# Kernel optimization log

Hardware: AMD Instinct MI355X
Metric: run time of the kernel (lower is better)

Reference implementation:

```python
import jax, jax.numpy as jnp
import numpy as np

B, C, H, W = 512, 32, 16, 16
HEADS = 8
D = C * H * W // HEADS  # 1024, per-head flattened dim; Linear is square (D -> D)
W_SCALE = 0.002


def setup_inputs() -> dict:
    key = jax.random.key(0)
    ks = jax.random.split(key, 9)
    f32 = jnp.float32
    return {
        "query": jax.random.normal(ks[0], (B, C, H, W), f32),
        "key": jax.random.normal(ks[1], (B, C, H, W), f32),
        "value": jax.random.normal(ks[2], (B, C, H, W), f32),
        # stacked per-head Linear params: W* is (heads, out=D, in=D) like torch Linear weight
        "W1": jax.random.normal(ks[3], (HEADS, D, D), f32) * W_SCALE,
        "b1": jax.random.normal(ks[4], (HEADS, D), f32) * W_SCALE,
        "W2": jax.random.normal(ks[5], (HEADS, D, D), f32) * W_SCALE,
        "b2": jax.random.normal(ks[6], (HEADS, D), f32) * W_SCALE,
        "W3": jax.random.normal(ks[7], (HEADS, D, D), f32) * W_SCALE,
        "b3": jax.random.normal(ks[8], (HEADS, D), f32) * W_SCALE,
    }


def reference(query, key, value, W1, b1, W2, b2, W3, b3):
    b, c, h, w = query.shape
    heads, d, _ = W1.shape
    # chunk over channels + flatten per head: (b, heads, d)
    q = query.reshape(b, heads, d)
    k = key.reshape(b, heads, d)
    v = value.reshape(b, heads, d)
    # per-head square Linear projections (torch: x @ W.T + b)
    q = jnp.einsum("nhd,hed->nhe", q, W1) + b1
    k = jnp.einsum("nhd,hed->nhe", k, W2) + b2
    v = jnp.einsum("nhd,hed->nhe", v, W3) + b3
    # original divides by p = 1/sqrt(d), i.e. multiplies scores by sqrt(d)
    scale = jnp.sqrt(jnp.asarray(d, q.dtype))
    scores = jnp.einsum("nhe,mhe->hnm", q, k) * scale  # (heads, b, b) attention over batch
    attn = jax.nn.softmax(scores, axis=-1)
    out = jnp.einsum("hnm,mhe->nhe", attn, v)  # (b, heads, d)
    return out.reshape(b, c, h, w)
```

## Files before the change

### kernel.cpp

```cpp
#include <hip/hip_runtime.h>

typedef _Float16 half8 __attribute__((ext_vector_type(8)));
typedef float f32x4 __attribute__((ext_vector_type(4)));

namespace {

constexpr int HEADS = 8;
constexpr int BATCH = 512;
constexpr int DH    = 1024;
constexpr int CHW   = HEADS * DH;

constexpr int BM = 128, BN = 128, BK = 32;
constexpr int LDW = BK + 8;

__device__ __forceinline__ int xcd_swz(int bid, int nwg) {
  const int q = nwg >> 3;
  return (bid & 7) * q + (bid >> 3);
}

__device__ __forceinline__ half8 cvt8(float4 a, float4 b) {
  half8 r;
  r[0] = (_Float16)a.x; r[1] = (_Float16)a.y; r[2] = (_Float16)a.z; r[3] = (_Float16)a.w;
  r[4] = (_Float16)b.x; r[5] = (_Float16)b.y; r[6] = (_Float16)b.z; r[7] = (_Float16)b.w;
  return r;
}

__global__ __launch_bounds__(256) void proj_kernel(
    const float* __restrict__ Xq, const float* __restrict__ Xk, const float* __restrict__ Xv,
    const float* __restrict__ W1, const float* __restrict__ b1,
    const float* __restrict__ W2, const float* __restrict__ b2,
    const float* __restrict__ W3, const float* __restrict__ b3,
    _Float16* __restrict__ Qp, _Float16* __restrict__ Kp, _Float16* __restrict__ VpT) {
  __shared__ _Float16 As[2][BM * LDW];
  __shared__ _Float16 Bs[2][BN * LDW];
  const int tid = threadIdx.x;
  const int l  = xcd_swz(blockIdx.x, 768);
  const int z  = l >> 8, rem = l & 255;
  const int h  = rem >> 5, bx = rem & 31;
  const int tm = bx & 3, tn = bx >> 2;
  const float* X    = (z == 0) ? Xq : (z == 1) ? Xk : Xv;
  const float* W    = (z == 0) ? W1 : (z == 1) ? W2 : W3;
  const float* bias = (z == 0) ? b1 : (z == 1) ? b2 : b3;
  _Float16*    P    = (z == 0) ? Qp : (z == 1) ? Kp : VpT;

  const int lane = tid & 63, w = tid >> 6;
  const int wr = (w >> 1) * 64, wc = (w & 1) * 64;
  const int lr = lane & 15, lk = lane >> 4;
  const int srow = tid >> 1, sc0 = (tid & 1) * 16;

  const float* ga = X + (size_t)(tm * BM + srow) * CHW + (size_t)h * DH + sc0;
  const float* gb = W + (size_t)h * DH * DH + (size_t)(tn * BN + srow) * DH + sc0;

  constexpr int NT = DH / BK;
  float4 ra0, ra1, ra2, ra3, rb0, rb1, rb2, rb3;
  ra0 = ((const float4*)ga)[0]; ra1 = ((const float4*)ga)[1];
  ra2 = ((const float4*)ga)[2]; ra3 = ((const float4*)ga)[3];
  rb0 = ((const float4*)gb)[0]; rb1 = ((const float4*)gb)[1];
  rb2 = ((const float4*)gb)[2]; rb3 = ((const float4*)gb)[3];
  ga += BK; gb += BK;
  *(half8*)&As[0][srow * LDW + sc0]     = cvt8(ra0, ra1);
  *(half8*)&As[0][srow * LDW + sc0 + 8] = cvt8(ra2, ra3);
  *(half8*)&Bs[0][srow * LDW + sc0]     = cvt8(rb0, rb1);
  *(half8*)&Bs[0][srow * LDW + sc0 + 8] = cvt8(rb2, rb3);
  ra0 = ((const float4*)ga)[0]; ra1 = ((const float4*)ga)[1];
  ra2 = ((const float4*)ga)[2]; ra3 = ((const float4*)ga)[3];
  rb0 = ((const float4*)gb)[0]; rb1 = ((const float4*)gb)[1];
  rb2 = ((const float4*)gb)[2]; rb3 = ((const float4*)gb)[3];
  ga += BK; gb += BK;
  __syncthreads();

  f32x4 acc[4][4] = {};
  int c = 0;
#pragma unroll 1
  for (int t = 0; t < NT; ++t) {
    const _Float16* Ac = As[c];
    const _Float16* Bc = Bs[c];
    half8 av[4], bv[4];
#pragma unroll
    for (int i = 0; i < 4; ++i)
      av[i] = *(const half8*)&Ac[(wr + i * 16 + lr) * LDW + lk * 8];
#pragma unroll
    for (int j = 0; j < 4; ++j)
      bv[j] = *(const half8*)&Bc[(wc + j * 16 + lr) * LDW + lk * 8];
    if (t + 1 < NT) {
      _Float16* An = As[c ^ 1];
      _Float16* Bn = Bs[c ^ 1];
      *(half8*)&An[srow * LDW + sc0]     = cvt8(ra0, ra1);
      *(half8*)&An[srow * LDW + sc0 + 8] = cvt8(ra2, ra3);
      *(half8*)&Bn[srow * LDW + sc0]     = cvt8(rb0, rb1);
      *(half8*)&Bn[srow * LDW + sc0 + 8] = cvt8(rb2, rb3);
      if (t + 2 < NT) {
        ra0 = ((const float4*)ga)[0]; ra1 = ((const float4*)ga)[1];
        ra2 = ((const float4*)ga)[2]; ra3 = ((const float4*)ga)[3];
        rb0 = ((const float4*)gb)[0]; rb1 = ((const float4*)gb)[1];
        rb2 = ((const float4*)gb)[2]; rb3 = ((const float4*)gb)[3];
        ga += BK; gb += BK;
      }
    }
#pragma unroll
    for (int i = 0; i < 4; ++i)
#pragma unroll
      for (int j = 0; j < 4; ++j)
        acc[i][j] = __builtin_amdgcn_mfma_f32_16x16x32_f16(av[i], bv[j], acc[i][j], 0, 0, 0);
    __syncthreads();
    c ^= 1;
  }

#pragma unroll
  for (int i = 0; i < 4; ++i)
#pragma unroll
    for (int j = 0; j < 4; ++j) {
      const int e = tn * BN + wc + j * 16 + lr;
      const float bb = bias[h * DH + e];
#pragma unroll
      for (int q = 0; q < 4; ++q) {
        const int n = tm * BM + wr + i * 16 + lk * 4 + q;
        const float val = acc[i][j][q] + bb;
        if (z != 2) P[((size_t)h * BATCH + n) * DH + e] = (_Float16)val;
        else        P[((size_t)h * DH + e) * BATCH + n] = (_Float16)val;
      }
    }
}

template <int NT>
__device__ __forceinline__ void gemm_f16_core(
    const _Float16* ga, const _Float16* gb,
    _Float16 (*As)[BM * LDW], _Float16 (*Bs)[BN * LDW],
    int srow, int sc0, int wr, int wc, int lr, int lk, f32x4 (&acc)[4][4]) {
  half8 rA0 = ((const half8*)ga)[0], rA1 = ((const half8*)ga)[1];
  half8 rB0 = ((const half8*)gb)[0], rB1 = ((const half8*)gb)[1];
  ga += BK; gb += BK;
  *(half8*)&As[0][srow * LDW + sc0]     = rA0;
  *(half8*)&As[0][srow * LDW + sc0 + 8] = rA1;
  *(half8*)&Bs[0][srow * LDW + sc0]     = rB0;
  *(half8*)&Bs[0][srow * LDW + sc0 + 8] = rB1;
  rA0 = ((const half8*)ga)[0]; rA1 = ((const half8*)ga)[1];
  rB0 = ((const half8*)gb)[0]; rB1 = ((const half8*)gb)[1];
  ga += BK; gb += BK;
  __syncthreads();

  int c = 0;
#pragma unroll 1
  for (int t = 0; t < NT; ++t) {
    const _Float16* Ac = As[c];
    const _Float16* Bc = Bs[c];
    half8 av[4], bv[4];
#pragma unroll
    for (int i = 0; i < 4; ++i)
      av[i] = *(const half8*)&Ac[(wr + i * 16 + lr) * LDW + lk * 8];
#pragma unroll
    for (int j = 0; j < 4; ++j)
      bv[j] = *(const half8*)&Bc[(wc + j * 16 + lr) * LDW + lk * 8];
    if (t + 1 < NT) {
      _Float16* An = As[c ^ 1];
      _Float16* Bn = Bs[c ^ 1];
      *(half8*)&An[srow * LDW + sc0]     = rA0;
      *(half8*)&An[srow * LDW + sc0 + 8] = rA1;
      *(half8*)&Bn[srow * LDW + sc0]     = rB0;
      *(half8*)&Bn[srow * LDW + sc0 + 8] = rB1;
      if (t + 2 < NT) {
        rA0 = ((const half8*)ga)[0]; rA1 = ((const half8*)ga)[1];
        rB0 = ((const half8*)gb)[0]; rB1 = ((const half8*)gb)[1];
        ga += BK; gb += BK;
      }
    }
#pragma unroll
    for (int i = 0; i < 4; ++i)
#pragma unroll
      for (int j = 0; j < 4; ++j)
        acc[i][j] = __builtin_amdgcn_mfma_f32_16x16x32_f16(av[i], bv[j], acc[i][j], 0, 0, 0);
    __syncthreads();
    c ^= 1;
  }
}

__global__ __launch_bounds__(256) void score_kernel(
    const _Float16* __restrict__ Qp, const _Float16* __restrict__ Kp,
    float* __restrict__ S) {
  __shared__ _Float16 As[2][BM * LDW];
  __shared__ _Float16 Bs[2][BN * LDW];
  const int tid = threadIdx.x;
  const int l  = xcd_swz(blockIdx.x, 128);
  const int h  = l >> 4, bx = l & 15;
  const int tm = bx & 3, tn = bx >> 2;
  const int lane = tid & 63, w = tid >> 6;
  const int wr = (w >> 1) * 64, wc = (w & 1) * 64;
  const int lr = lane & 15, lk = lane >> 4;
  const int srow = tid >> 1, sc0 = (tid & 1) * 16;

  const _Float16* ga = Qp + ((size_t)h * BATCH + tm * BM + srow) * DH + sc0;
  const _Float16* gb = Kp + ((size_t)h * BATCH + tn * BN + srow) * DH + sc0;

  f32x4 acc[4][4] = {};
  gemm_f16_core<DH / BK>(ga, gb, As, Bs, srow, sc0, wr, wc, lr, lk, acc);

#pragma unroll
  for (int i = 0; i < 4; ++i)
#pragma unroll
    for (int j = 0; j < 4; ++j) {
      const int m = tn * BN + wc + j * 16 + lr;
#pragma unroll
      for (int q = 0; q < 4; ++q) {
        const int n = tm * BM + wr + i * 16 + lk * 4 + q;
        S[((size_t)h * BATCH + n) * BATCH + m] = 32.0f * acc[i][j][q];
      }
    }
}

__global__ __launch_bounds__(64) void softmax_kernel(
    const float* __restrict__ S, _Float16* __restrict__ A) {
  const size_t r = (size_t)blockIdx.x * BATCH;
  const int l = threadIdx.x;
  float v[8];
  float mx = -1e30f;
#pragma unroll
  for (int i = 0; i < 8; ++i) { v[i] = S[r + i * 64 + l]; mx = fmaxf(mx, v[i]); }
#pragma unroll
  for (int off = 32; off; off >>= 1) mx = fmaxf(mx, __shfl_xor(mx, off));
  float sum = 0.f;
#pragma unroll
  for (int i = 0; i < 8; ++i) { v[i] = __expf(v[i] - mx); sum += v[i]; }
#pragma unroll
  for (int off = 32; off; off >>= 1) sum += __shfl_xor(sum, off);
  const float inv = 1.f / sum;
#pragma unroll
  for (int i = 0; i < 8; ++i) A[r + i * 64 + l] = (_Float16)(v[i] * inv);
}

__global__ __launch_bounds__(256) void pv_kernel(
    const _Float16* __restrict__ At, const _Float16* __restrict__ VpT,
    float* __restrict__ Out) {
  __shared__ _Float16 As[2][BM * LDW];
  __shared__ _Float16 Bs[2][BN * LDW];
  const int tid = threadIdx.x;
  const int l  = xcd_swz(blockIdx.x, 256);
  const int h  = l >> 5, bx = l & 31;
  const int tm = bx & 3, tn = bx >> 2;
  const int lane = tid & 63, w = tid >> 6;
  const int wr = (w >> 1) * 64, wc = (w & 1) * 64;
  const int lr = lane & 15, lk = lane >> 4;
  const int srow = tid >> 1, sc0 = (tid & 1) * 16;

  const _Float16* ga = At  + ((size_t)h * BATCH + tm * BM + srow) * BATCH + sc0;
  const _Float16* gb = VpT + ((size_t)h * DH   + tn * BN + srow) * BATCH + sc0;

  f32x4 acc[4][4] = {};
  gemm_f16_core<BATCH / BK>(ga, gb, As, Bs, srow, sc0, wr, wc, lr, lk, acc);

#pragma unroll
  for (int i = 0; i < 4; ++i)
#pragma unroll
    for (int j = 0; j < 4; ++j) {
      const int e = tn * BN + wc + j * 16 + lr;
#pragma unroll
      for (int q = 0; q < 4; ++q) {
        const int n = tm * BM + wr + i * 16 + lk * 4 + q;
        Out[((size_t)n * HEADS + h) * DH + e] = acc[i][j][q];
      }
    }
}

}

extern "C" void kernel_launch(void* const* d_in, const int* in_sizes, int n_in,
                              void* d_out, int out_size, void* d_ws, size_t ws_size,
                              hipStream_t stream) {
  (void)in_sizes; (void)n_in; (void)out_size; (void)ws_size;
  const float* q  = (const float*)d_in[0];
  const float* k  = (const float*)d_in[1];
  const float* v  = (const float*)d_in[2];
  const float* W1 = (const float*)d_in[3];
  const float* b1 = (const float*)d_in[4];
  const float* W2 = (const float*)d_in[5];
  const float* b2 = (const float*)d_in[6];
  const float* W3 = (const float*)d_in[7];
  const float* b3 = (const float*)d_in[8];
  float* out = (float*)d_out;

  _Float16* Qp  = (_Float16*)d_ws;
  _Float16* Kp  = Qp + (size_t)BATCH * HEADS * DH;
  _Float16* VpT = Kp + (size_t)BATCH * HEADS * DH;
  float*    S   = (float*)(VpT + (size_t)BATCH * HEADS * DH);
  _Float16* At  = (_Float16*)(S + (size_t)HEADS * BATCH * BATCH);

  const dim3 blk(256);
  proj_kernel<<<dim3(768), blk, 0, stream>>>(q, k, v, W1, b1, W2, b2, W3, b3, Qp, Kp, VpT);
  score_kernel<<<dim3(128), blk, 0, stream>>>(Qp, Kp, S);
  softmax_kernel<<<dim3(HEADS * BATCH), dim3(64), 0, stream>>>(S, At);
  pv_kernel<<<dim3(256), blk, 0, stream>>>(At, VpT, out);
}
```

Before: 108.2 us.

## Use direct global-to-LDS loads with XOR-swizzled single-buffer tiles in all GEMMs

Replaces the register-staged, double-buffered LDS fill in the projection, score and PV GEMMs with global_load_lds 16-byte direct copies into an XOR-swizzled single-buffer tile. The projection kernel now stores fp32 tiles in LDS and converts to fp16 when reading fragments. The fp16 GEMMs move to a K tile of 64 with two MFMAs per fragment pair. This is meant to cut VGPR staging, LDS bank conflicts and loop overhead. In exchange it loses the overlap of the next tile's global load with compute, since each iteration loads then waits behind two barriers.

```diff
diff --git a/kernel.cpp b/kernel.cpp
--- a/kernel.cpp
+++ b/kernel.cpp
@@ -10,12 +10,17 @@
 constexpr int DH    = 1024;
 constexpr int CHW   = HEADS * DH;
 
-constexpr int BM = 128, BN = 128, BK = 32;
-constexpr int LDW = BK + 8;
+constexpr int BM = 128, BN = 128;
 
 __device__ __forceinline__ int xcd_swz(int bid, int nwg) {
   const int q = nwg >> 3;
   return (bid & 7) * q + (bid >> 3);
+}
+
+typedef __attribute__((address_space(3))) unsigned int lds_u32;
+typedef const __attribute__((address_space(1))) unsigned int glb_u32;
+__device__ __forceinline__ void gl_lds16(const void* g, void* l) {
+  __builtin_amdgcn_global_load_lds((glb_u32*)g, (lds_u32*)l, 16, 0, 0);
 }
 
 __device__ __forceinline__ half8 cvt8(float4 a, float4 b) {
@@ -31,8 +36,8 @@
     const float* __restrict__ W2, const float* __restrict__ b2,
     const float* __restrict__ W3, const float* __restrict__ b3,
     _Float16* __restrict__ Qp, _Float16* __restrict__ Kp, _Float16* __restrict__ VpT) {
-  __shared__ _Float16 As[2][BM * LDW];
-  __shared__ _Float16 Bs[2][BN * LDW];
+  __shared__ __align__(16) float As[BM * 32];
+  __shared__ __align__(16) float Bs[BN * 32];
   const int tid = threadIdx.x;
   const int l  = xcd_swz(blockIdx.x, 768);
   const int z  = l >> 8, rem = l & 255;
@@ -46,64 +51,57 @@
   const int lane = tid & 63, w = tid >> 6;
   const int wr = (w >> 1) * 64, wc = (w & 1) * 64;
   const int lr = lane & 15, lk = lane >> 4;
-  const int srow = tid >> 1, sc0 = (tid & 1) * 16;
-
-  const float* ga = X + (size_t)(tm * BM + srow) * CHW + (size_t)h * DH + sc0;
-  const float* gb = W + (size_t)h * DH * DH + (size_t)(tn * BN + srow) * DH + sc0;
-
-  constexpr int NT = DH / BK;
-  float4 ra0, ra1, ra2, ra3, rb0, rb1, rb2, rb3;
-  ra0 = ((const float4*)ga)[0]; ra1 = ((const float4*)ga)[1];
-  ra2 = ((const float4*)ga)[2]; ra3 = ((const float4*)ga)[3];
-  rb0 = ((const float4*)gb)[0]; rb1 = ((const float4*)gb)[1];
-  rb2 = ((const float4*)gb)[2]; rb3 = ((const float4*)gb)[3];
-  ga += BK; gb += BK;
-  *(half8*)&As[0][srow * LDW + sc0]     = cvt8(ra0, ra1);
-  *(half8*)&As[0][srow * LDW + sc0 + 8] = cvt8(ra2, ra3);
-  *(half8*)&Bs[0][srow * LDW + sc0]     = cvt8(rb0, rb1);
-  *(half8*)&Bs[0][srow * LDW + sc0 + 8] = cvt8(rb2, rb3);
-  ra0 = ((const float4*)ga)[0]; ra1 = ((const float4*)ga)[1];
-  ra2 = ((const float4*)ga)[2]; ra3 = ((const float4*)ga)[3];
-  rb0 = ((const float4*)gb)[0]; rb1 = ((const float4*)gb)[1];
-  rb2 = ((const float4*)gb)[2]; rb3 = ((const float4*)gb)[3];
-  ga += BK; gb += BK;
-  __syncthreads();
-
+
+  const char* Ab = (const char*)(X + (size_t)tm * BM * CHW + (size_t)h * DH);
+  const char* Bb = (const char*)(W + (size_t)h * DH * DH + (size_t)tn * BN * DH);
+
+  const char* srcA0; const char* srcA1; const char* srcA2; const char* srcA3;
+  const char* srcB0; const char* srcB1; const char* srcB2; const char* srcB3;
+  int off0, off1, off2, off3;
+  {
+    int off, row, scb;
+    off = 0 * 4096 + tid * 16; row = off >> 7; scb = ((off >> 4) & 7) ^ (row & 7);
+    off0 = off; srcA0 = Ab + (size_t)row * (CHW * 4) + scb * 16; srcB0 = Bb + (size_t)row * (DH * 4) + scb * 16;
+    off = 1 * 4096 + tid * 16; row = off >> 7; scb = ((off >> 4) & 7) ^ (row & 7);
+    off1 = off; srcA1 = Ab + (size_t)row * (CHW * 4) + scb * 16; srcB1 = Bb + (size_t)row * (DH * 4) + scb * 16;
+    off = 2 * 4096 + tid * 16; row = off >> 7; scb = ((off >> 4) & 7) ^ (row & 7);
+    off2 = off; srcA2 = Ab + (size_t)row * (CHW * 4) + scb * 16; srcB2 = Bb + (size_t)row * (DH * 4) + scb * 16;
+    off = 3 * 4096 + tid * 16; row = off >> 7; scb = ((off >> 4) & 7) ^ (row & 7);
+    off3 = off; srcA3 = Ab + (size_t)row * (CHW * 4) + scb * 16; srcB3 = Bb + (size_t)row * (DH * 4) + scb * 16;
+  }
+
+  constexpr int NT = DH / 32;
   f32x4 acc[4][4] = {};
-  int c = 0;
 #pragma unroll 1
   for (int t = 0; t < NT; ++t) {
-    const _Float16* Ac = As[c];
-    const _Float16* Bc = Bs[c];
+    __syncthreads();
+    gl_lds16(srcA0, (char*)As + off0); gl_lds16(srcB0, (char*)Bs + off0);
+    gl_lds16(srcA1, (char*)As + off1); gl_lds16(srcB1, (char*)Bs + off1);
+    gl_lds16(srcA2, (char*)As + off2); gl_lds16(srcB2, (char*)Bs + off2);
+    gl_lds16(srcA3, (char*)As + off3); gl_lds16(srcB3, (char*)Bs + off3);
+    srcA0 += 128; srcA1 += 128; srcA2 += 128; srcA3 += 128;
+    srcB0 += 128; srcB1 += 128; srcB2 += 128; srcB3 += 128;
+    __syncthreads();
     half8 av[4], bv[4];
 #pragma unroll
-    for (int i = 0; i < 4; ++i)
-      av[i] = *(const half8*)&Ac[(wr + i * 16 + lr) * LDW + lk * 8];
-#pragma unroll
-    for (int j = 0; j < 4; ++j)
-      bv[j] = *(const half8*)&Bc[(wc + j * 16 + lr) * LDW + lk * 8];
-    if (t + 1 < NT) {
-      _Float16* An = As[c ^ 1];
-      _Float16* Bn = Bs[c ^ 1];
-      *(half8*)&An[srow * LDW + sc0]     = cvt8(ra0, ra1);
-      *(half8*)&An[srow * LDW + sc0 + 8] = cvt8(ra2, ra3);
-      *(half8*)&Bn[srow * LDW + sc0]     = cvt8(rb0, rb1);
-      *(half8*)&Bn[srow * LDW + sc0 + 8] = cvt8(rb2, rb3);
-      if (t + 2 < NT) {
-        ra0 = ((const float4*)ga)[0]; ra1 = ((const float4*)ga)[1];
-        ra2 = ((const float4*)ga)[2]; ra3 = ((const float4*)ga)[3];
-        rb0 = ((const float4*)gb)[0]; rb1 = ((const float4*)gb)[1];
-        rb2 = ((const float4*)gb)[2]; rb3 = ((const float4*)gb)[3];
-        ga += BK; gb += BK;
-      }
+    for (int i = 0; i < 4; ++i) {
+      const int row = wr + i * 16 + lr;
+      const float4 p0 = *(const float4*)&As[row * 32 + (((lk * 2)    ) ^ (row & 7)) * 4];
+      const float4 p1 = *(const float4*)&As[row * 32 + (((lk * 2 + 1)) ^ (row & 7)) * 4];
+      av[i] = cvt8(p0, p1);
+    }
+#pragma unroll
+    for (int j = 0; j < 4; ++j) {
+      const int row = wc + j * 16 + lr;
+      const float4 p0 = *(const float4*)&Bs[row * 32 + (((lk * 2)    ) ^ (row & 7)) * 4];
+      const float4 p1 = *(const float4*)&Bs[row * 32 + (((lk * 2 + 1)) ^ (row & 7)) * 4];
+      bv[j] = cvt8(p0, p1);
     }
 #pragma unroll
     for (int i = 0; i < 4; ++i)
 #pragma unroll
       for (int j = 0; j < 4; ++j)
         acc[i][j] = __builtin_amdgcn_mfma_f32_16x16x32_f16(av[i], bv[j], acc[i][j], 0, 0, 0);
-    __syncthreads();
-    c ^= 1;
   }
 
 #pragma unroll
@@ -123,62 +121,63 @@
 }
 
 template <int NT>
-__device__ __forceinline__ void gemm_f16_core(
-    const _Float16* ga, const _Float16* gb,
-    _Float16 (*As)[BM * LDW], _Float16 (*Bs)[BN * LDW],
-    int srow, int sc0, int wr, int wc, int lr, int lk, f32x4 (&acc)[4][4]) {
-  half8 rA0 = ((const half8*)ga)[0], rA1 = ((const half8*)ga)[1];
-  half8 rB0 = ((const half8*)gb)[0], rB1 = ((const half8*)gb)[1];
-  ga += BK; gb += BK;
-  *(half8*)&As[0][srow * LDW + sc0]     = rA0;
-  *(half8*)&As[0][srow * LDW + sc0 + 8] = rA1;
-  *(half8*)&Bs[0][srow * LDW + sc0]     = rB0;
-  *(half8*)&Bs[0][srow * LDW + sc0 + 8] = rB1;
-  rA0 = ((const half8*)ga)[0]; rA1 = ((const half8*)ga)[1];
-  rB0 = ((const half8*)gb)[0]; rB1 = ((const half8*)gb)[1];
-  ga += BK; gb += BK;
-  __syncthreads();
-
-  int c = 0;
+__device__ __forceinline__ void gemm16_core(
+    const char* ga, size_t lda, const char* gb, size_t ldb,
+    _Float16* As, _Float16* Bs,
+    int tid, int wr, int wc, int lr, int lk, f32x4 (&acc)[4][4]) {
+  const char* srcA0; const char* srcA1; const char* srcA2; const char* srcA3;
+  const char* srcB0; const char* srcB1; const char* srcB2; const char* srcB3;
+  int off0, off1, off2, off3;
+  {
+    int off, row, scb;
+    off = 0 * 4096 + tid * 16; row = off >> 7; scb = ((off >> 4) & 7) ^ (row & 7);
+    off0 = off; srcA0 = ga + (size_t)row * lda + scb * 16; srcB0 = gb + (size_t)row * ldb + scb * 16;
+    off = 1 * 4096 + tid * 16; row = off >> 7; scb = ((off >> 4) & 7) ^ (row & 7);
+    off1 = off; srcA1 = ga + (size_t)row * lda + scb * 16; srcB1 = gb + (size_t)row * ldb + scb * 16;
+    off = 2 * 4096 + tid * 16; row = off >> 7; scb = ((off >> 4) & 7) ^ (row & 7);
+    off2 = off; srcA2 = ga + (size_t)row * lda + scb * 16; srcB2 = gb + (size_t)row * ldb + scb * 16;
+    off = 3 * 4096 + tid * 16; row = off >> 7; scb = ((off >> 4) & 7) ^ (row & 7);
+    off3 = off; srcA3 = ga + (size_t)row * lda + scb * 16; srcB3 = gb + (size_t)row * ldb + scb * 16;
+  }
+
 #pragma unroll 1
   for (int t = 0; t < NT; ++t) {
-    const _Float16* Ac = As[c];
-    const _Float16* Bc = Bs[c];
-    half8 av[4], bv[4];
+    __syncthreads();
+    gl_lds16(srcA0, (char*)As + off0); gl_lds16(srcB0, (char*)Bs + off0);
+    gl_lds16(srcA1, (char*)As + off1); gl_lds16(srcB1, (char*)Bs + off1);
+    gl_lds16(srcA2, (char*)As + off2); gl_lds16(srcB2, (char*)Bs + off2);
+    gl_lds16(srcA3, (char*)As + off3); gl_lds16(srcB3, (char*)Bs + off3);
+    srcA0 += 128; srcA1 += 128; srcA2 += 128; srcA3 += 128;
+    srcB0 += 128; srcB1 += 128; srcB2 += 128; srcB3 += 128;
+    __syncthreads();
+    half8 a0[4], a1[4], b0[4], b1[4];
+#pragma unroll
+    for (int i = 0; i < 4; ++i) {
+      const int row = wr + i * 16 + lr;
+      a0[i] = *(const half8*)&As[row * 64 + ((lk    ) ^ (row & 7)) * 8];
+      a1[i] = *(const half8*)&As[row * 64 + ((4 + lk) ^ (row & 7)) * 8];
+    }
+#pragma unroll
+    for (int j = 0; j < 4; ++j) {
+      const int row = wc + j * 16 + lr;
+      b0[j] = *(const half8*)&Bs[row * 64 + ((lk    ) ^ (row & 7)) * 8];
+      b1[j] = *(const half8*)&Bs[row * 64 + ((4 + lk) ^ (row & 7)) * 8];
+    }
 #pragma unroll
     for (int i = 0; i < 4; ++i)
-      av[i] = *(const half8*)&Ac[(wr + i * 16 + lr) * LDW + lk * 8];
-#pragma unroll
-    for (int j = 0; j < 4; ++j)
-      bv[j] = *(const half8*)&Bc[(wc + j * 16 + lr) * LDW + lk * 8];
-    if (t + 1 < NT) {
-      _Float16* An = As[c ^ 1];
-      _Float16* Bn = Bs[c ^ 1];
-      *(half8*)&An[srow * LDW + sc0]     = rA0;
-      *(half8*)&An[srow * LDW + sc0 + 8] = rA1;
-      *(half8*)&Bn[srow * LDW + sc0]     = rB0;
-      *(half8*)&Bn[srow * LDW + sc0 + 8] = rB1;
-      if (t + 2 < NT) {
-        rA0 = ((const half8*)ga)[0]; rA1 = ((const half8*)ga)[1];
-        rB0 = ((const half8*)gb)[0]; rB1 = ((const half8*)gb)[1];
-        ga += BK; gb += BK;
-      }
-    }
-#pragma unroll
-    for (int i = 0; i < 4; ++i)
-#pragma unroll
-      for (int j = 0; j < 4; ++j)
-        acc[i][j] = __builtin_amdgcn_mfma_f32_16x16x32_f16(av[i], bv[j], acc[i][j], 0, 0, 0);
-    __syncthreads();
-    c ^= 1;
+#pragma unroll
+      for (int j = 0; j < 4; ++j) {
+        acc[i][j] = __builtin_amdgcn_mfma_f32_16x16x32_f16(a0[i], b0[j], acc[i][j], 0, 0, 0);
+        acc[i][j] = __builtin_amdgcn_mfma_f32_16x16x32_f16(a1[i], b1[j], acc[i][j], 0, 0, 0);
+      }
   }
 }
 
 __global__ __launch_bounds__(256) void score_kernel(
     const _Float16* __restrict__ Qp, const _Float16* __restrict__ Kp,
     float* __restrict__ S) {
-  __shared__ _Float16 As[2][BM * LDW];
-  __shared__ _Float16 Bs[2][BN * LDW];
+  __shared__ __align__(16) _Float16 As[BM * 64];
+  __shared__ __align__(16) _Float16 Bs[BN * 64];
   const int tid = threadIdx.x;
   const int l  = xcd_swz(blockIdx.x, 128);
   const int h  = l >> 4, bx = l & 15;
@@ -186,13 +185,12 @@
   const int lane = tid & 63, w = tid >> 6;
   const int wr = (w >> 1) * 64, wc = (w & 1) * 64;
   const int lr = lane & 15, lk = lane >> 4;
-  const int srow = tid >> 1, sc0 = (tid & 1) * 16;
-
-  const _Float16* ga = Qp + ((size_t)h * BATCH + tm * BM + srow) * DH + sc0;
-  const _Float16* gb = Kp + ((size_t)h * BATCH + tn * BN + srow) * DH + sc0;
+
+  const char* ga = (const char*)(Qp + ((size_t)h * BATCH + tm * BM) * DH);
+  const char* gb = (const char*)(Kp + ((size_t)h * BATCH + tn * BN) * DH);
 
   f32x4 acc[4][4] = {};
-  gemm_f16_core<DH / BK>(ga, gb, As, Bs, srow, sc0, wr, wc, lr, lk, acc);
+  gemm16_core<DH / 64>(ga, DH * 2, gb, DH * 2, As, Bs, tid, wr, wc, lr, lk, acc);
 
 #pragma unroll
   for (int i = 0; i < 4; ++i)
@@ -230,8 +228,8 @@
 __global__ __launch_bounds__(256) void pv_kernel(
     const _Float16* __restrict__ At, const _Float16* __restrict__ VpT,
     float* __restrict__ Out) {
-  __shared__ _Float16 As[2][BM * LDW];
-  __shared__ _Float16 Bs[2][BN * LDW];
+  __shared__ __align__(16) _Float16 As[BM * 64];
+  __shared__ __align__(16) _Float16 Bs[BN * 64];
   const int tid = threadIdx.x;
   const int l  = xcd_swz(blockIdx.x, 256);
   const int h  = l >> 5, bx = l & 31;
@@ -239,13 +237,12 @@
   const int lane = tid & 63, w = tid >> 6;
   const int wr = (w >> 1) * 64, wc = (w & 1) * 64;
   const int lr = lane & 15, lk = lane >> 4;
-  const int srow = tid >> 1, sc0 = (tid & 1) * 16;
-
-  const _Float16* ga = At  + ((size_t)h * BATCH + tm * BM + srow) * BATCH + sc0;
-  const _Float16* gb = VpT + ((size_t)h * DH   + tn * BN + srow) * BATCH + sc0;
+
+  const char* ga = (const char*)(At  + ((size_t)h * BATCH + tm * BM) * BATCH);
+  const char* gb = (const char*)(VpT + ((size_t)h * DH   + tn * BN) * BATCH);
 
   f32x4 acc[4][4] = {};
-  gemm_f16_core<BATCH / BK>(ga, gb, As, Bs, srow, sc0, wr, wc, lr, lk, acc);
+  gemm16_core<BATCH / 64>(ga, BATCH * 2, gb, BATCH * 2, As, Bs, tid, wr, wc, lr, lk, acc);
 
 #pragma unroll
   for (int i = 0; i < 4; ++i)
```

Result: no change. 108.5 us (+0.3%).
